# Optimization experiments

Hardware: AMD Instinct MI355X
Metric: run time of the kernel (lower is better)

Reference implementation:

```python
import jax, jax.numpy as jnp
import numpy as np

N_NODES = 100000
N_EDGES = 600000
VOCAB = 50000
EMBED_DIM = 128
HIDDEN_DIM = 128


def gcn_conv(h, W, b, src, dst, n_nodes):
    """PyG GCNConv: x' = D^{-1/2} (A+I) D^{-1/2} X W + b.
    src/dst already include self-loops."""
    hw = h @ W                                   # [N, out]
    deg = jnp.zeros((n_nodes,), hw.dtype).at[dst].add(1.0)   # in-degree incl. self-loop
    dinv = jax.lax.rsqrt(deg)                    # deg >= 1 thanks to self-loops
    norm = dinv[src] * dinv[dst]                 # [E+N]
    msgs = norm[:, None] * hw[src]               # gather [E+N, out]
    out = jnp.zeros_like(hw).at[dst].add(msgs)   # scatter-aggregate
    return out + b


def setup_inputs() -> dict:
    key = jax.random.key(0)
    ks = jax.random.split(key, 8)
    x = jax.random.randint(ks[0], (N_NODES,), 0, VOCAB, dtype=jnp.int64 if jax.config.jax_enable_x64 else jnp.int32)
    edge_index = jax.random.randint(ks[1], (2, N_EDGES), 0, N_NODES, dtype=jnp.int32)
    emb = jax.random.normal(ks[2], (VOCAB, EMBED_DIM), dtype=jnp.float32)
    # Glorot-style scale for GCN weights
    W1 = jax.random.normal(ks[3], (EMBED_DIM, HIDDEN_DIM), dtype=jnp.float32) * (1.0 / np.sqrt(EMBED_DIM))
    b1 = jnp.zeros((HIDDEN_DIM,), dtype=jnp.float32)
    W2 = jax.random.normal(ks[4], (HIDDEN_DIM, HIDDEN_DIM), dtype=jnp.float32) * (1.0 / np.sqrt(HIDDEN_DIM))
    b2 = jnp.zeros((HIDDEN_DIM,), dtype=jnp.float32)
    return {"x": x, "edge_index": edge_index, "emb": emb, "W1": W1, "b1": b1, "W2": W2, "b2": b2}


def reference(x, edge_index, emb, W1, b1, W2, b2):
    n = x.shape[0]
    loops = jnp.arange(n, dtype=edge_index.dtype)
    src = jnp.concatenate([edge_index[0], loops])  # add self-loops once
    dst = jnp.concatenate([edge_index[1], loops])
    h = emb[x]                                     # [N, embed_dim] embedding lookup
    h = jax.nn.relu(gcn_conv(h, W1, b1, src, dst, n))
    h = jax.nn.relu(gcn_conv(h, W2, b2, src, dst, n))
    return h
```

## Files before the change

### kernel.cpp

```cpp
#include <hip/hip_runtime.h>


#define NDIM 128
#define PAD_K 136
#define SCAN_IPT 4
#define SCAN_BLK 256
#define SCAN_IPB (SCAN_BLK * SCAN_IPT)

typedef __bf16 bf16x8 __attribute__((ext_vector_type(8)));
typedef __bf16 bf16x4 __attribute__((ext_vector_type(4)));
typedef float f32x4 __attribute__((ext_vector_type(4)));

__device__ __forceinline__ float bf2f(unsigned short u) {
    union { unsigned int i; float f; } c;
    c.i = (unsigned int)u << 16;
    return c.f;
}
__device__ __forceinline__ unsigned short f2bf(float f) {
    __bf16 b = (__bf16)f;
    return __builtin_bit_cast(unsigned short, b);
}

__global__ void degree_count(const int* __restrict__ dst, int* __restrict__ cnt, int E) {
    int e = blockIdx.x * blockDim.x + threadIdx.x;
    if (e < E) atomicAdd(&cnt[dst[e]], 1);
}

__global__ void scan_blocks(const int* __restrict__ in, int* __restrict__ out,
                            int* __restrict__ bsums, int n) {
    __shared__ int lds[SCAN_BLK];
    const int t = threadIdx.x;
    const int base = blockIdx.x * SCAN_IPB + t * SCAN_IPT;
    int v[SCAN_IPT];
    int s = 0;
#pragma unroll
    for (int k = 0; k < SCAN_IPT; ++k) { v[k] = (base + k < n) ? in[base + k] : 0; s += v[k]; }
    lds[t] = s;
    __syncthreads();
    for (int off = 1; off < SCAN_BLK; off <<= 1) {
        int x = (t >= off) ? lds[t - off] : 0;
        __syncthreads();
        lds[t] += x;
        __syncthreads();
    }
    if (t == SCAN_BLK - 1) bsums[blockIdx.x] = lds[t];
    int run = (t == 0) ? 0 : lds[t - 1];
#pragma unroll
    for (int k = 0; k < SCAN_IPT; ++k) {
        if (base + k < n) out[base + k] = run;
        run += v[k];
    }
}

__global__ void scan_partials(int* __restrict__ bsums, int nb) {
    __shared__ int lds[128];
    const int t = threadIdx.x;
    lds[t] = (t < nb) ? bsums[t] : 0;
    __syncthreads();
    for (int off = 1; off < 128; off <<= 1) {
        int x = (t >= off) ? lds[t - off] : 0;
        __syncthreads();
        lds[t] += x;
        __syncthreads();
    }
    if (t < nb) bsums[t] = (t == 0) ? 0 : lds[t - 1];
}

__global__ void add_offsets_dinv(int* __restrict__ rp, const int* __restrict__ bsums,
                                 const int* __restrict__ cnt, float* __restrict__ dinv,
                                 int n, int E) {
    int i = blockIdx.x * blockDim.x + threadIdx.x;
    if (i < n) {
        rp[i] += bsums[i / SCAN_IPB];
        dinv[i] = rsqrtf((float)cnt[i] + 1.0f);
    }
    if (i == 0) rp[n] = E;
}

__global__ void fill_edges(const int* __restrict__ src, const int* __restrict__ dst,
                           const int* __restrict__ rp, int* __restrict__ cur,
                           int* __restrict__ esrc, int E) {
    int e = blockIdx.x * blockDim.x + threadIdx.x;
    if (e >= E) return;
    int d = dst[e];
    int p = rp[d] + atomicAdd(&cur[d], 1);
    esrc[p] = src[e];
}

__global__ void wt_convert2(const float* __restrict__ W1, const float* __restrict__ W2,
                            unsigned short* __restrict__ WT1, unsigned short* __restrict__ WT2) {
    int c = blockIdx.x * blockDim.x + threadIdx.x;
    int cc = c & 16383;
    int j = cc >> 7, k = cc & 127;
    if (c < 16384) WT1[cc] = f2bf(W1[k * 128 + j]);
    else           WT2[cc] = f2bf(W2[k * 128 + j]);
}

template <int MODE>
__global__ __launch_bounds__(256, 2)
void gemm_mfma(const void* __restrict__ Hsrc, const int* __restrict__ idx,
               const unsigned short* __restrict__ WTb, const float* __restrict__ dinv,
               unsigned short* __restrict__ outb, int n) {
    __shared__ __bf16 sA[128 * PAD_K];
    __shared__ __bf16 sBT[128 * PAD_K];
    const int tid = threadIdx.x;
    const int rbase = blockIdx.x * 128;

    {
        const uint4* src = (const uint4*)WTb;
#pragma unroll
        for (int i = 0; i < 8; ++i) {
            int c = tid + i * 256;
            int j = c >> 4, u = c & 15;
            *(uint4*)&sBT[j * PAD_K + u * 8] = src[c];
        }
    }
    if (MODE == 0) {
        const float* H = (const float*)Hsrc;
#pragma unroll
        for (int i = 0; i < 16; ++i) {
            int c = tid + i * 256;
            int r = c >> 5, c4 = c & 31;
            int gr = rbase + r;
            int srow = (gr < n) ? idx[gr] : 0;
            float4 v = ((const float4*)H)[(size_t)srow * 32 + c4];
            bf16x4 w = { (__bf16)v.x, (__bf16)v.y, (__bf16)v.z, (__bf16)v.w };
            *(bf16x4*)&sA[r * PAD_K + c4 * 4] = w;
        }
    } else {
        const unsigned short* H = (const unsigned short*)Hsrc;
#pragma unroll
        for (int i = 0; i < 8; ++i) {
            int c = tid + i * 256;
            int r = c >> 4, u = c & 15;
            int gr = rbase + r;
            int srow = (gr < n) ? gr : 0;
            uint4 v = ((const uint4*)(H + (size_t)srow * 128))[u];
            *(uint4*)&sA[r * PAD_K + u * 8] = v;
        }
    }
    __syncthreads();

    const int wave = tid >> 6, lane = tid & 63;
    const int quad = lane >> 4, lrow = lane & 15;

    f32x4 acc[2][8];
#pragma unroll
    for (int mt = 0; mt < 2; ++mt)
#pragma unroll
        for (int nt = 0; nt < 8; ++nt) acc[mt][nt] = (f32x4)0.0f;

#pragma unroll
    for (int ks = 0; ks < 4; ++ks) {
        const int kb = ks * 32 + quad * 8;
        bf16x8 a0 = *(const bf16x8*)&sA[(wave * 32 + lrow) * PAD_K + kb];
        bf16x8 a1 = *(const bf16x8*)&sA[(wave * 32 + 16 + lrow) * PAD_K + kb];
#pragma unroll
        for (int nt = 0; nt < 8; ++nt) {
            bf16x8 b = *(const bf16x8*)&sBT[(nt * 16 + lrow) * PAD_K + kb];
            acc[0][nt] = __builtin_amdgcn_mfma_f32_16x16x32_bf16(a0, b, acc[0][nt], 0, 0, 0);
            acc[1][nt] = __builtin_amdgcn_mfma_f32_16x16x32_bf16(a1, b, acc[1][nt], 0, 0, 0);
        }
    }

#pragma unroll
    for (int mt = 0; mt < 2; ++mt) {
#pragma unroll
        for (int r = 0; r < 4; ++r) {
            int grow = rbase + wave * 32 + mt * 16 + quad * 4 + r;
            if (grow < n) {
                float dsc = dinv[grow];
                unsigned short* orow = outb + (size_t)grow * NDIM + lrow;
#pragma unroll
                for (int nt = 0; nt < 8; ++nt)
                    orow[nt * 16] = f2bf(dsc * acc[mt][nt][r]);
            }
        }
    }
}

template <bool OUT_BF16>
__global__ void aggregate_csr(const unsigned short* __restrict__ vs, const int* __restrict__ rp,
                              const int* __restrict__ esrc, const float* __restrict__ dinv,
                              const float* __restrict__ bias, void* __restrict__ out, int n) {
    int t = blockIdx.x * blockDim.x + threadIdx.x;
    int i = t >> 5, lane = t & 31;
    if (i >= n) return;
    const ushort4* vs4 = (const ushort4*)vs;
    ushort4 u = vs4[(size_t)i * 32 + lane];
    float4 acc = make_float4(bf2f(u.x), bf2f(u.y), bf2f(u.z), bf2f(u.w));
    int j = rp[i];
    const int end = rp[i + 1];
    for (; j + 4 <= end; j += 4) {
        int s0 = esrc[j], s1 = esrc[j + 1], s2 = esrc[j + 2], s3 = esrc[j + 3];
        ushort4 v0 = vs4[(size_t)s0 * 32 + lane];
        ushort4 v1 = vs4[(size_t)s1 * 32 + lane];
        ushort4 v2 = vs4[(size_t)s2 * 32 + lane];
        ushort4 v3 = vs4[(size_t)s3 * 32 + lane];
        acc.x += (bf2f(v0.x) + bf2f(v1.x)) + (bf2f(v2.x) + bf2f(v3.x));
        acc.y += (bf2f(v0.y) + bf2f(v1.y)) + (bf2f(v2.y) + bf2f(v3.y));
        acc.z += (bf2f(v0.z) + bf2f(v1.z)) + (bf2f(v2.z) + bf2f(v3.z));
        acc.w += (bf2f(v0.w) + bf2f(v1.w)) + (bf2f(v2.w) + bf2f(v3.w));
    }
    for (; j < end; ++j) {
        int s = esrc[j];
        ushort4 v = vs4[(size_t)s * 32 + lane];
        acc.x += bf2f(v.x);
        acc.y += bf2f(v.y);
        acc.z += bf2f(v.z);
        acc.w += bf2f(v.w);
    }
    float di = dinv[i];
    float4 b = ((const float4*)bias)[lane];
    acc.x = fmaxf(fmaf(di, acc.x, b.x), 0.0f);
    acc.y = fmaxf(fmaf(di, acc.y, b.y), 0.0f);
    acc.z = fmaxf(fmaf(di, acc.z, b.z), 0.0f);
    acc.w = fmaxf(fmaf(di, acc.w, b.w), 0.0f);
    if (OUT_BF16) {
        ushort4 o = make_ushort4(f2bf(acc.x), f2bf(acc.y), f2bf(acc.z), f2bf(acc.w));
        ((ushort4*)out)[(size_t)i * 32 + lane] = o;
    } else {
        ((float4*)out)[(size_t)i * 32 + lane] = acc;
    }
}

extern "C" void kernel_launch(void* const* d_in, const int* in_sizes, int n_in,
                              void* d_out, int out_size, void* d_ws, size_t ws_size,
                              hipStream_t stream) {
    const int* x = (const int*)d_in[0];
    const int* edge_index = (const int*)d_in[1];
    const float* emb = (const float*)d_in[2];
    const float* W1 = (const float*)d_in[3];
    const float* b1 = (const float*)d_in[4];
    const float* W2 = (const float*)d_in[5];
    const float* b2 = (const float*)d_in[6];
    float* out = (float*)d_out;

    const int N = in_sizes[0];
    const int E = in_sizes[1] / 2;
    const int* src = edge_index;
    const int* dst = edge_index + E;

    char* p = (char*)d_ws;
    auto alloc = [&](size_t bytes) {
        char* q = p;
        p += (bytes + 511) & ~(size_t)511;
        return q;
    };
    int* cnt = (int*)alloc((size_t)2 * N * sizeof(int));
    int* cur = cnt + N;
    int* rp = (int*)alloc((size_t)(N + 1) * sizeof(int));
    float* dinv = (float*)alloc((size_t)N * sizeof(float));
    int* bsums = (int*)alloc(128 * sizeof(int));
    int* esrc = (int*)alloc((size_t)E * sizeof(int));
    unsigned short* WT1 = (unsigned short*)alloc(16384 * sizeof(unsigned short));
    unsigned short* WT2 = (unsigned short*)alloc(16384 * sizeof(unsigned short));
    unsigned short* hwb = (unsigned short*)alloc((size_t)N * NDIM * sizeof(unsigned short));
    unsigned short* h1b = (unsigned short*)alloc((size_t)N * NDIM * sizeof(unsigned short));
    (void)ws_size;

    const int NB = (N + SCAN_IPB - 1) / SCAN_IPB;

    hipMemsetAsync(cnt, 0, (size_t)2 * N * sizeof(int), stream);
    degree_count<<<(E + 255) / 256, 256, 0, stream>>>(dst, cnt, E);
    scan_blocks<<<NB, SCAN_BLK, 0, stream>>>(cnt, rp, bsums, N);
    scan_partials<<<1, 128, 0, stream>>>(bsums, NB);
    add_offsets_dinv<<<(N + 255) / 256, 256, 0, stream>>>(rp, bsums, cnt, dinv, N, E);
    fill_edges<<<(E + 255) / 256, 256, 0, stream>>>(src, dst, rp, cur, esrc, E);

    wt_convert2<<<128, 256, 0, stream>>>(W1, W2, WT1, WT2);

    const int gemm_blocks = (N + 127) / 128;
    const int agg_blocks = (int)(((size_t)N * 32 + 255) / 256);

    gemm_mfma<0><<<gemm_blocks, 256, 0, stream>>>(emb, x, WT1, dinv, hwb, N);
    aggregate_csr<true><<<agg_blocks, 256, 0, stream>>>(hwb, rp, esrc, dinv, b1, h1b, N);
    gemm_mfma<1><<<gemm_blocks, 256, 0, stream>>>(h1b, nullptr, WT2, dinv, hwb, N);
    aggregate_csr<false><<<agg_blocks, 256, 0, stream>>>(hwb, rp, esrc, dinv, b2, out, N);
}
```

Baseline: 275.8 us.

## Precompute embedding-table times W1 then gather rows instead of gathering then GEMM

Uses (emb[x])@W1 = (emb@W1)[x] to run the first GEMM over the 50k-row vocabulary table instead of the 100k gathered node rows, then adds a gather_scale kernel that picks rows and applies dinv. The GEMM tile also shrinks from 128 to 64 rows with launch bounds raised to 3 blocks per SM, and a SCALE template flag skips the dinv multiply. This halves the first GEMM's work but adds an extra kernel launch and another N×128 bf16 round trip through memory. The gathered values are also rounded to bf16 twice.

```diff
diff --git a/kernel.cpp b/kernel.cpp
--- a/kernel.cpp
+++ b/kernel.cpp
@@ -96,47 +96,46 @@
     else           WT2[cc] = f2bf(W2[k * 128 + j]);
 }
 
-template <int MODE>
-__global__ __launch_bounds__(256, 2)
-void gemm_mfma(const void* __restrict__ Hsrc, const int* __restrict__ idx,
-               const unsigned short* __restrict__ WTb, const float* __restrict__ dinv,
-               unsigned short* __restrict__ outb, int n) {
-    __shared__ __bf16 sA[128 * PAD_K];
+template <int MODE, bool SCALE>
+__global__ __launch_bounds__(256, 3)
+void gemm_mfma(const void* __restrict__ Asrc, const unsigned short* __restrict__ WTb,
+               const float* __restrict__ dinv, unsigned short* __restrict__ outb, int n) {
+    __shared__ __bf16 sA[64 * PAD_K];
     __shared__ __bf16 sBT[128 * PAD_K];
     const int tid = threadIdx.x;
-    const int rbase = blockIdx.x * 128;
-
+    const int rbase = blockIdx.x * 64;
+
+    if (MODE == 0) {
+        const float* A = (const float*)Asrc;
+#pragma unroll
+        for (int i = 0; i < 8; ++i) {
+            int c = tid + i * 256;
+            int r = c >> 5, c4 = c & 31;
+            int gr = rbase + r;
+            int srow = (gr < n) ? gr : (n - 1);
+            float4 v = ((const float4*)A)[(size_t)srow * 32 + c4];
+            bf16x4 w = { (__bf16)v.x, (__bf16)v.y, (__bf16)v.z, (__bf16)v.w };
+            *(bf16x4*)&sA[r * PAD_K + c4 * 4] = w;
+        }
+    } else {
+        const unsigned short* A = (const unsigned short*)Asrc;
+#pragma unroll
+        for (int i = 0; i < 4; ++i) {
+            int c = tid + i * 256;
+            int r = c >> 4, u = c & 15;
+            int gr = rbase + r;
+            int srow = (gr < n) ? gr : (n - 1);
+            uint4 v = ((const uint4*)(A + (size_t)srow * 128))[u];
+            *(uint4*)&sA[r * PAD_K + u * 8] = v;
+        }
+    }
     {
-        const uint4* src = (const uint4*)WTb;
+        const uint4* bsrc = (const uint4*)WTb;
 #pragma unroll
         for (int i = 0; i < 8; ++i) {
             int c = tid + i * 256;
             int j = c >> 4, u = c & 15;
-            *(uint4*)&sBT[j * PAD_K + u * 8] = src[c];
-        }
-    }
-    if (MODE == 0) {
-        const float* H = (const float*)Hsrc;
-#pragma unroll
-        for (int i = 0; i < 16; ++i) {
-            int c = tid + i * 256;
-            int r = c >> 5, c4 = c & 31;
-            int gr = rbase + r;
-            int srow = (gr < n) ? idx[gr] : 0;
-            float4 v = ((const float4*)H)[(size_t)srow * 32 + c4];
-            bf16x4 w = { (__bf16)v.x, (__bf16)v.y, (__bf16)v.z, (__bf16)v.w };
-            *(bf16x4*)&sA[r * PAD_K + c4 * 4] = w;
-        }
-    } else {
-        const unsigned short* H = (const unsigned short*)Hsrc;
-#pragma unroll
-        for (int i = 0; i < 8; ++i) {
-            int c = tid + i * 256;
-            int r = c >> 4, u = c & 15;
-            int gr = rbase + r;
-            int srow = (gr < n) ? gr : 0;
-            uint4 v = ((const uint4*)(H + (size_t)srow * 128))[u];
-            *(uint4*)&sA[r * PAD_K + u * 8] = v;
+            *(uint4*)&sBT[j * PAD_K + u * 8] = bsrc[c];
         }
     }
     __syncthreads();
@@ -144,39 +143,47 @@
     const int wave = tid >> 6, lane = tid & 63;
     const int quad = lane >> 4, lrow = lane & 15;
 
-    f32x4 acc[2][8];
-#pragma unroll
-    for (int mt = 0; mt < 2; ++mt)
-#pragma unroll
-        for (int nt = 0; nt < 8; ++nt) acc[mt][nt] = (f32x4)0.0f;
+    f32x4 acc[8];
+#pragma unroll
+    for (int nt = 0; nt < 8; ++nt) acc[nt] = (f32x4)0.0f;
 
 #pragma unroll
     for (int ks = 0; ks < 4; ++ks) {
         const int kb = ks * 32 + quad * 8;
-        bf16x8 a0 = *(const bf16x8*)&sA[(wave * 32 + lrow) * PAD_K + kb];
-        bf16x8 a1 = *(const bf16x8*)&sA[(wave * 32 + 16 + lrow) * PAD_K + kb];
+        bf16x8 a = *(const bf16x8*)&sA[(wave * 16 + lrow) * PAD_K + kb];
 #pragma unroll
         for (int nt = 0; nt < 8; ++nt) {
             bf16x8 b = *(const bf16x8*)&sBT[(nt * 16 + lrow) * PAD_K + kb];
-            acc[0][nt] = __builtin_amdgcn_mfma_f32_16x16x32_bf16(a0, b, acc[0][nt], 0, 0, 0);
-            acc[1][nt] = __builtin_amdgcn_mfma_f32_16x16x32_bf16(a1, b, acc[1][nt], 0, 0, 0);
-        }
-    }
-
-#pragma unroll
-    for (int mt = 0; mt < 2; ++mt) {
-#pragma unroll
-        for (int r = 0; r < 4; ++r) {
-            int grow = rbase + wave * 32 + mt * 16 + quad * 4 + r;
-            if (grow < n) {
-                float dsc = dinv[grow];
-                unsigned short* orow = outb + (size_t)grow * NDIM + lrow;
-#pragma unroll
-                for (int nt = 0; nt < 8; ++nt)
-                    orow[nt * 16] = f2bf(dsc * acc[mt][nt][r]);
-            }
-        }
-    }
+            acc[nt] = __builtin_amdgcn_mfma_f32_16x16x32_bf16(a, b, acc[nt], 0, 0, 0);
+        }
+    }
+
+#pragma unroll
+    for (int r = 0; r < 4; ++r) {
+        int grow = rbase + wave * 16 + quad * 4 + r;
+        if (grow < n) {
+            float dsc = SCALE ? dinv[grow] : 1.0f;
+            unsigned short* orow = outb + (size_t)grow * NDIM + lrow;
+#pragma unroll
+            for (int nt = 0; nt < 8; ++nt)
+                orow[nt * 16] = f2bf(SCALE ? dsc * acc[nt][r] : acc[nt][r]);
+        }
+    }
+}
+
+__global__ void gather_scale(const unsigned short* __restrict__ tab, const int* __restrict__ x,
+                             const float* __restrict__ dinv, unsigned short* __restrict__ vs,
+                             int n) {
+    int t = blockIdx.x * blockDim.x + threadIdx.x;
+    int i = t >> 4, u = t & 15;
+    if (i >= n) return;
+    int row = x[i];
+    float di = dinv[i];
+    union { uint4 q; unsigned short s[8]; } a;
+    a.q = ((const uint4*)(tab + (size_t)row * 128))[u];
+#pragma unroll
+    for (int k = 0; k < 8; ++k) a.s[k] = f2bf(di * bf2f(a.s[k]));
+    ((uint4*)(vs + (size_t)i * 128))[u] = a.q;
 }
 
 template <bool OUT_BF16>
@@ -238,6 +245,7 @@
 
     const int N = in_sizes[0];
     const int E = in_sizes[1] / 2;
+    const int V = in_sizes[2] / NDIM;
     const int* src = edge_index;
     const int* dst = edge_index + E;
 
@@ -255,8 +263,10 @@
     int* esrc = (int*)alloc((size_t)E * sizeof(int));
     unsigned short* WT1 = (unsigned short*)alloc(16384 * sizeof(unsigned short));
     unsigned short* WT2 = (unsigned short*)alloc(16384 * sizeof(unsigned short));
-    unsigned short* hwb = (unsigned short*)alloc((size_t)N * NDIM * sizeof(unsigned short));
+    unsigned short* embW1 = (unsigned short*)alloc((size_t)V * NDIM * sizeof(unsigned short));
+    unsigned short* vs1 = (unsigned short*)alloc((size_t)N * NDIM * sizeof(unsigned short));
     unsigned short* h1b = (unsigned short*)alloc((size_t)N * NDIM * sizeof(unsigned short));
+    unsigned short* vs2 = (unsigned short*)alloc((size_t)N * NDIM * sizeof(unsigned short));
     (void)ws_size;
 
     const int NB = (N + SCAN_IPB - 1) / SCAN_IPB;
@@ -270,11 +280,12 @@
 
     wt_convert2<<<128, 256, 0, stream>>>(W1, W2, WT1, WT2);
 
-    const int gemm_blocks = (N + 127) / 128;
     const int agg_blocks = (int)(((size_t)N * 32 + 255) / 256);
-
-    gemm_mfma<0><<<gemm_blocks, 256, 0, stream>>>(emb, x, WT1, dinv, hwb, N);
-    aggregate_csr<true><<<agg_blocks, 256, 0, stream>>>(hwb, rp, esrc, dinv, b1, h1b, N);
-    gemm_mfma<1><<<gemm_blocks, 256, 0, stream>>>(h1b, nullptr, WT2, dinv, hwb, N);
-    aggregate_csr<false><<<agg_blocks, 256, 0, stream>>>(hwb, rp, esrc, dinv, b2, out, N);
-}
+    const int gs_blocks = (int)(((size_t)N * 16 + 255) / 256);
+
+    gemm_mfma<0, false><<<(V + 63) / 64, 256, 0, stream>>>(emb, WT1, nullptr, embW1, V);
+    gather_scale<<<gs_blocks, 256, 0, stream>>>(embW1, x, dinv, vs1, N);
+    aggregate_csr<true><<<agg_blocks, 256, 0, stream>>>(vs1, rp, esrc, dinv, b1, h1b, N);
+    gemm_mfma<1, true><<<(N + 63) / 64, 256, 0, stream>>>(h1b, WT2, dinv, vs2, N);
+    aggregate_csr<false><<<agg_blocks, 256, 0, stream>>>(vs2, rp, esrc, dinv, b2, out, N);
+}
```

Result: faster. 258.4 us (-6.3%).
